# Kernel tuning notes

Measured on AMD Instinct MI355X. Metric: run time of the kernel, lower is better.

Reference implementation:

```python
import jax, jax.numpy as jnp
import numpy as np

N = 4096      # mesh nodes (seq len)
D = 512       # input_dim_nodes / hidden_size
F = 512       # ffn_hidden_size (hidden_dim)
NH = 4        # num_attention_heads
HD = D // NH  # head dim = 128
L = 2         # processor_layers
EPS = 1e-5
SCALE = 1.0 / float(np.sqrt(HD))
NEG = -1e9


def setup_inputs() -> dict:
    key = jax.random.key(0)
    ks = jax.random.split(key, 16)
    nfeat = jax.random.normal(ks[0], (N, D), jnp.float32)
    # sparse graph adjacency mask: True = masked out (TE 'arbitrary' convention)
    mask = jax.random.uniform(ks[1], (N, N)) < 0.99
    idx = jnp.arange(N)
    mask = mask.at[idx, idx].set(False)  # keep self-edges unmasked
    s = 0.02
    p = lambda k, shape: jax.random.normal(k, shape, jnp.float32) * s
    return dict(
        nfeat=nfeat, mask=mask,
        ln1_g=jnp.ones((L, D), jnp.float32), ln1_b=jnp.zeros((L, D), jnp.float32),
        wq=p(ks[2], (L, D, D)), bq=p(ks[3], (L, D)),
        wk=p(ks[4], (L, D, D)), bk=p(ks[5], (L, D)),
        wv=p(ks[6], (L, D, D)), bv=p(ks[7], (L, D)),
        wo=p(ks[8], (L, D, D)), bo=p(ks[9], (L, D)),
        ln2_g=jnp.ones((L, D), jnp.float32), ln2_b=jnp.zeros((L, D), jnp.float32),
        fc1_w=p(ks[10], (L, F, D)), fc1_b=p(ks[11], (L, F)),
        fc2_w=p(ks[12], (L, D, F)), fc2_b=p(ks[13], (L, D)),
    )


def _ln(x, g, b):
    mu = x.mean(-1, keepdims=True)
    var = ((x - mu) ** 2).mean(-1, keepdims=True)
    return (x - mu) * jax.lax.rsqrt(var + EPS) * g + b


def reference(nfeat, mask, ln1_g, ln1_b, wq, bq, wk, bk, wv, bv, wo, bo,
              ln2_g, ln2_b, fc1_w, fc1_b, fc2_w, fc2_b):
    def layer(x, p):
        g1, b1, Wq, Bq, Wk, Bk, Wv, Bv, Wo, Bo, g2, b2, W1, B1, W2, B2 = p
        # --- pre-LN self-attention with arbitrary mask ---
        h = _ln(x, g1, b1)                                  # [N, D]
        q = (h @ Wq.T + Bq).reshape(N, NH, HD)
        k = (h @ Wk.T + Bk).reshape(N, NH, HD)
        v = (h @ Wv.T + Bv).reshape(N, NH, HD)
        scores = jnp.einsum('qhd,khd->hqk', q, k) * SCALE   # [NH, N, N]
        scores = jnp.where(mask[None], NEG, scores)
        attn = jax.nn.softmax(scores, axis=-1)
        o = jnp.einsum('hqk,khd->qhd', attn, v).reshape(N, D)
        x = x + o @ Wo.T + Bo
        # --- pre-LN MLP ---
        h2 = _ln(x, g2, b2)
        m = jax.nn.gelu(h2 @ W1.T + B1, approximate=False) @ W2.T + B2
        return x + m, None

    xs = (ln1_g, ln1_b, wq, bq, wk, bk, wv, bv, wo, bo,
          ln2_g, ln2_b, fc1_w, fc1_b, fc2_w, fc2_b)
    out, _ = jax.lax.scan(layer, nfeat, xs)
    return out
```

## Files before the change

### kernel.cpp

```cpp
#include <hip/hip_runtime.h>
#include <math.h>

#define NN 4096
#define DD 512
#define FF 512
#define CAP 256
#define SCALE 0.08838834764831845f

typedef __attribute__((ext_vector_type(8))) short short8;
typedef __attribute__((ext_vector_type(8))) unsigned short ushort8;
typedef __attribute__((ext_vector_type(4))) float floatx4;

__device__ __forceinline__ float bf2f(unsigned short u) {
    union { unsigned int i; float f; } x; x.i = ((unsigned int)u) << 16; return x.f;
}
__device__ __forceinline__ unsigned short f2bf(float f) {
    union { float f; unsigned int i; } x; x.f = f;
    unsigned int r = (x.i + 0x7FFFu + ((x.i >> 16) & 1u)) >> 16;
    return (unsigned short)r;
}
__device__ __forceinline__ void gld_lds16(const void* g, void* l) {
    __builtin_amdgcn_global_load_lds((const __attribute__((address_space(1))) void*)g,
                                     (__attribute__((address_space(3))) void*)l, 16, 0, 0);
}

__global__ void build_idx_kernel(const int* __restrict__ mask,
                                 int* __restrict__ idx, int* __restrict__ cnt) {
    int row = blockIdx.x;
    __shared__ int c;
    if (threadIdx.x == 0) c = 0;
    __syncthreads();
    const int4* mrow = (const int4*)(mask + (size_t)row * NN);
    for (int j4 = threadIdx.x; j4 < NN / 4; j4 += blockDim.x) {
        int4 m4 = mrow[j4];
        int base = j4 * 4;
        if (m4.x == 0) idx[row * CAP + atomicAdd(&c, 1)] = base;
        if (m4.y == 0) idx[row * CAP + atomicAdd(&c, 1)] = base + 1;
        if (m4.z == 0) idx[row * CAP + atomicAdd(&c, 1)] = base + 2;
        if (m4.w == 0) idx[row * CAP + atomicAdd(&c, 1)] = base + 3;
    }
    __syncthreads();
    if (threadIdx.x == 0) cnt[row] = (c < CAP) ? c : CAP;
}

struct FoldArgs {
    const float* w[6];
    const float* bias[6];
    const float* ln1_g; const float* ln1_b;
    const float* ln2_g; const float* ln2_b;
};
__global__ void fold_weights(FoldArgs fa, unsigned short* __restrict__ wc,
                             float* __restrict__ c0, float* __restrict__ c1) {
    int r = blockIdx.y;
    int l = r / 6, m = r - l * 6;
    int wave = threadIdx.x >> 6, lane = threadIdx.x & 63;
    int n = blockIdx.x * 4 + wave;

    const float* wrow = fa.w[m] + (size_t)l * DD * DD + (size_t)n * DD;
    float4 w0 = *(const float4*)&wrow[lane * 8];
    float4 w1 = *(const float4*)&wrow[lane * 8 + 4];
    float we[8] = {w0.x, w0.y, w0.z, w0.w, w1.x, w1.y, w1.z, w1.w};

    bool folded = (m < 3) || (m == 4);
    float s1 = 0.f, sb = 0.f;
    float wg[8];
    if (folded) {
        const float* gp = (m < 3) ? fa.ln1_g + l * DD : fa.ln2_g + l * DD;
        const float* bp = (m < 3) ? fa.ln1_b + l * DD : fa.ln2_b + l * DD;
        float4 g0 = *(const float4*)&gp[lane * 8];
        float4 g1 = *(const float4*)&gp[lane * 8 + 4];
        float4 b0 = *(const float4*)&bp[lane * 8];
        float4 b1 = *(const float4*)&bp[lane * 8 + 4];
        float ge[8] = {g0.x, g0.y, g0.z, g0.w, g1.x, g1.y, g1.z, g1.w};
        float be[8] = {b0.x, b0.y, b0.z, b0.w, b1.x, b1.y, b1.z, b1.w};
#pragma unroll
        for (int e = 0; e < 8; e++) {
            wg[e] = we[e] * ge[e];
            s1 += wg[e];
            sb += we[e] * be[e];
        }
    } else {
#pragma unroll
        for (int e = 0; e < 8; e++) wg[e] = we[e];
    }
    ushort8 ov;
#pragma unroll
    for (int e = 0; e < 8; e++) ov[e] = f2bf(wg[e]);
    *(ushort8*)&wc[(size_t)r * DD * DD + (size_t)n * DD + lane * 8] = ov;

    if (folded) {
#pragma unroll
        for (int off = 32; off; off >>= 1) { s1 += __shfl_xor(s1, off); sb += __shfl_xor(sb, off); }
    }
    if (lane == 0) {
        c1[r * DD + n] = folded ? s1 : 0.f;
        c0[r * DD + n] = (folded ? sb : 0.f) + fa.bias[m][l * DD + n];
    }
}

__global__ void init_stats(const float* __restrict__ x, unsigned short* __restrict__ xb,
                           float* __restrict__ S) {
    int wave = threadIdx.x >> 6, lane = threadIdx.x & 63;
    int row = blockIdx.x * 4 + wave;
    const float* xr = x + (size_t)row * DD;
    float4 p0 = *(const float4*)&xr[lane * 8];
    float4 p1 = *(const float4*)&xr[lane * 8 + 4];
    float v[8] = {p0.x, p0.y, p0.z, p0.w, p1.x, p1.y, p1.z, p1.w};
    float s = 0.f, q = 0.f;
    ushort8 ov;
#pragma unroll
    for (int e = 0; e < 8; e++) { s += v[e]; q += v[e] * v[e]; ov[e] = f2bf(v[e]); }
#pragma unroll
    for (int off = 32; off; off >>= 1) { s += __shfl_xor(s, off); q += __shfl_xor(q, off); }
    *(ushort8*)&xb[(size_t)row * DD + lane * 8] = ov;
    if (lane == 0) { S[2 * row] = s; S[2 * row + 1] = q; }
}

__global__ void zero_kernel(float* __restrict__ p, int n) {
    int i = blockIdx.x * blockDim.x + threadIdx.x;
    if (i < n) p[i] = 0.f;
}

template <int MODE>
__launch_bounds__(256)
__global__ void gemm_bf16(const unsigned short* __restrict__ A, const unsigned short* __restrict__ B,
                          const float* __restrict__ c0, const float* __restrict__ c1,
                          const float* __restrict__ statsIn, const float* __restrict__ resIn,
                          float* __restrict__ resOut, unsigned short* __restrict__ outB,
                          float* __restrict__ statsOut, int M, int Nout, int K) {
    __shared__ unsigned short As[64 * 32];
    __shared__ unsigned short Bs[64 * 32];
    const int m0 = blockIdx.y * 64, n0 = blockIdx.x * 64;
    const int t = threadIdx.x;
    const int wave = t >> 6, lane = t & 63;
    const int wm = (wave & 1) * 32, wn = (wave >> 1) * 32;
    const int srow = t >> 2, scol = (t & 3) * 8;
    const int fr = lane & 15, fq = (lane >> 4) * 8;

    floatx4 acc[2][2] = {};

    const unsigned short* ag = A + (size_t)(m0 + srow) * K + scol;
    const unsigned short* bg = B + (size_t)(n0 + srow) * K + scol;
    unsigned short* as = As + t * 8;
    unsigned short* bs = Bs + t * 8;

    for (int k0 = 0; k0 < K; k0 += 32) {
        __syncthreads();
        gld_lds16(ag + k0, as);
        gld_lds16(bg + k0, bs);
        __syncthreads();
        short8 af[2], bf[2];
#pragma unroll
        for (int i = 0; i < 2; i++)
            af[i] = *(const short8*)&As[(wm + 16 * i + fr) * 32 + fq];
#pragma unroll
        for (int j = 0; j < 2; j++)
            bf[j] = *(const short8*)&Bs[(wn + 16 * j + fr) * 32 + fq];
#pragma unroll
        for (int i = 0; i < 2; i++)
#pragma unroll
            for (int j = 0; j < 2; j++)
                acc[i][j] = __builtin_amdgcn_mfma_f32_16x16x32_bf16(af[i], bf[j], acc[i][j], 0, 0, 0);
    }

    const int er = (lane >> 4) * 4, ec = lane & 15;
    int colj[2]; float c0v[2], c1v[2];
#pragma unroll
    for (int j = 0; j < 2; j++) {
        colj[j] = n0 + wn + 16 * j + ec;
        c0v[j] = c0[colj[j]];
        if (MODE < 2) c1v[j] = c1[colj[j]];
    }

#pragma unroll
    for (int i = 0; i < 2; i++) {
#pragma unroll
        for (int r = 0; r < 4; r++) {
            int row = m0 + wm + 16 * i + er + r;
            if (MODE < 2) {
                float s = statsIn[2 * row], q = statsIn[2 * row + 1];
                float mu = s * (1.0f / DD);
                float var = q * (1.0f / DD) - mu * mu;
                float rm = rsqrtf(var + 1e-5f);
                float rmu = rm * mu;
#pragma unroll
                for (int j = 0; j < 2; j++) {
                    float val = rm * acc[i][j][r] - rmu * c1v[j] + c0v[j];
                    if (MODE == 1) val = 0.5f * val * (1.0f + erff(val * 0.70710678118654752f));
                    outB[(size_t)row * Nout + colj[j]] = f2bf(val);
                }
            } else {
                float xn[2];
#pragma unroll
                for (int j = 0; j < 2; j++) {
                    xn[j] = resIn[(size_t)row * Nout + colj[j]] + acc[i][j][r] + c0v[j];
                    resOut[(size_t)row * Nout + colj[j]] = xn[j];
                    if (MODE == 2) outB[(size_t)row * Nout + colj[j]] = f2bf(xn[j]);
                }
                if (MODE == 2) {
                    float s = xn[0] + xn[1];
                    float q = xn[0] * xn[0] + xn[1] * xn[1];
#pragma unroll
                    for (int off = 1; off < 16; off <<= 1) {
                        s += __shfl_xor(s, off);
                        q += __shfl_xor(q, off);
                    }
                    if ((lane & 15) == 0) {
                        atomicAdd(&statsOut[2 * row], s);
                        atomicAdd(&statsOut[2 * row + 1], q);
                    }
                }
            }
        }
    }
}

__global__ void sparse_attn(const unsigned short* __restrict__ qkv, const int* __restrict__ idx,
                            const int* __restrict__ cnt, unsigned short* __restrict__ o) {
    int wave = threadIdx.x >> 6, lane = threadIdx.x & 63;
    int qslot = wave >> 1, half = wave & 1;
    int qi = blockIdx.x * 4 + qslot;
    __shared__ float obuf[4][64][8];
    __shared__ float sbuf[4][64];

    ushort8 qv = *(const ushort8*)(qkv + (size_t)qi * 1536 + lane * 8);
    float qf[8];
#pragma unroll
    for (int e = 0; e < 8; e++) qf[e] = bf2f(qv[e]);

    int c = cnt[qi];
    const int* ir = idx + qi * CAP;
    float sum = 0.f, oa[8] = {};

    for (int j = half; j < c; j += 2) {
        int kj = ir[j];
        const unsigned short* kv_base = qkv + (size_t)kj * 1536;
        ushort8 kv = *(const ushort8*)(kv_base + 512 + lane * 8);
        ushort8 vv = *(const ushort8*)(kv_base + 1024 + lane * 8);
        float d = 0.f;
#pragma unroll
        for (int e = 0; e < 8; e++) d += qf[e] * bf2f(kv[e]);
        d += __shfl_xor(d, 1);
        d += __shfl_xor(d, 2);
        d += __shfl_xor(d, 4);
        d += __shfl_xor(d, 8);
        float p = __expf(d * SCALE);
        sum += p;
#pragma unroll
        for (int e = 0; e < 8; e++) oa[e] += p * bf2f(vv[e]);
    }

    if (half == 1) {
#pragma unroll
        for (int e = 0; e < 8; e++) obuf[qslot][lane][e] = oa[e];
        sbuf[qslot][lane] = sum;
    }
    __syncthreads();
    if (half == 0) {
        sum += sbuf[qslot][lane];
        float inv = 1.0f / sum;
        ushort8 ov;
#pragma unroll
        for (int e = 0; e < 8; e++) ov[e] = f2bf((oa[e] + obuf[qslot][lane][e]) * inv);
        *(ushort8*)(o + (size_t)qi * 512 + lane * 8) = ov;
    }
}

extern "C" void kernel_launch(void* const* d_in, const int* in_sizes, int n_in,
                              void* d_out, int out_size, void* d_ws, size_t ws_size,
                              hipStream_t stream) {
    const float* nfeat = (const float*)d_in[0];
    const int*   mask  = (const int*)d_in[1];
    const float* ln1_g = (const float*)d_in[2];
    const float* ln1_b = (const float*)d_in[3];
    const float* wq    = (const float*)d_in[4];
    const float* bq    = (const float*)d_in[5];
    const float* wk    = (const float*)d_in[6];
    const float* bk    = (const float*)d_in[7];
    const float* wv    = (const float*)d_in[8];
    const float* bv    = (const float*)d_in[9];
    const float* wo    = (const float*)d_in[10];
    const float* bo    = (const float*)d_in[11];
    const float* ln2_g = (const float*)d_in[12];
    const float* ln2_b = (const float*)d_in[13];
    const float* fc1_w = (const float*)d_in[14];
    const float* fc1_b = (const float*)d_in[15];
    const float* fc2_w = (const float*)d_in[16];
    const float* fc2_b = (const float*)d_in[17];

    const size_t ND = (size_t)NN * DD;
    float* x            = (float*)d_ws;
    unsigned short* xb  = (unsigned short*)(x + ND);
    unsigned short* qkv = xb + ND;
    unsigned short* o   = qkv + (size_t)NN * 1536;
    unsigned short* m1  = o + ND;
    unsigned short* wc  = m1 + ND;
    float* c0           = (float*)(wc + (size_t)12 * DD * DD);
    float* c1           = c0 + 12 * DD;
    float* S            = c1 + 12 * DD;
    int*   idx          = (int*)(S + 4 * NN * 2);
    int*   cnt          = idx + (size_t)NN * CAP;

    FoldArgs fa;
    fa.w[0] = wq; fa.w[1] = wk; fa.w[2] = wv; fa.w[3] = wo; fa.w[4] = fc1_w; fa.w[5] = fc2_w;
    fa.bias[0] = bq; fa.bias[1] = bk; fa.bias[2] = bv; fa.bias[3] = bo; fa.bias[4] = fc1_b; fa.bias[5] = fc2_b;
    fa.ln1_g = ln1_g; fa.ln1_b = ln1_b; fa.ln2_g = ln2_g; fa.ln2_b = ln2_b;

    fold_weights<<<dim3(128, 12), 256, 0, stream>>>(fa, wc, c0, c1);
    build_idx_kernel<<<NN, 256, 0, stream>>>(mask, idx, cnt);
    init_stats<<<NN / 4, 256, 0, stream>>>(nfeat, xb, S);
    zero_kernel<<<24, 1024, 0, stream>>>(S + NN * 2, 3 * NN * 2);

    for (int l = 0; l < 2; l++) {
        unsigned short* wl = wc + (size_t)l * 6 * DD * DD;
        float* cl0 = c0 + l * 6 * DD;
        float* cl1 = c1 + l * 6 * DD;
        float* Sa = S + (size_t)(2 * l) * NN * 2;
        float* Sb = S + (size_t)(2 * l + 1) * NN * 2;
        const float* resIn0 = (l == 0) ? nfeat : x;

        gemm_bf16<0><<<dim3(24, 64), 256, 0, stream>>>(xb, wl, cl0, cl1, Sa,
                                                       nullptr, nullptr, qkv, nullptr, NN, 1536, DD);
        sparse_attn<<<NN / 4, 512, 0, stream>>>(qkv, idx, cnt, o);
        gemm_bf16<2><<<dim3(8, 64), 256, 0, stream>>>(o, wl + (size_t)3 * DD * DD, cl0 + 3 * DD, nullptr,
                                                      nullptr, resIn0, x, xb, Sb, NN, DD, DD);
        gemm_bf16<1><<<dim3(8, 64), 256, 0, stream>>>(xb, wl + (size_t)4 * DD * DD, cl0 + 4 * DD, cl1 + 4 * DD, Sb,
                                                      nullptr, nullptr, m1, nullptr, NN, FF, DD);
        if (l == 0) {
            gemm_bf16<2><<<dim3(8, 64), 256, 0, stream>>>(m1, wl + (size_t)5 * DD * DD, cl0 + 5 * DD, nullptr,
                                                          nullptr, x, x, xb, S + (size_t)2 * NN * 2, NN, DD, FF);
        } else {
            gemm_bf16<3><<<dim3(8, 64), 256, 0, stream>>>(m1, wl + (size_t)5 * DD * DD, cl0 + 5 * DD, nullptr,
                                                          nullptr, x, (float*)d_out, nullptr, nullptr, NN, DD, FF);
        }
    }
}
```

Baseline: 321.8 us.

## Fuse all stages into one cooperative persistent kernel with grid syncs

Replaces the chain of separate launches (weight fold, mask indexing, stats init, zeroing, GEMMs, attention) with one cooperative kernel of 512 blocks that walks every stage and separates them with grid.sync(). Row statistics are no longer accumulated with global atomics. Each GEMM column block writes partial sums to a buffer, and the next GEMM reduces them when it loads its LayerNorm coefficients into shared memory, which also removes the zeroing kernel. The aim is to cut launch and tail overhead. The cost is less parallelism in the QKV GEMM (1536 tiles on 512 blocks) and attention, plus the grid-wide barriers themselves. A multi-launch fallback runs if the cooperative launch fails.

```diff
diff --git a/kernel.cpp b/kernel.cpp
--- a/kernel.cpp
+++ b/kernel.cpp
@@ -1,5 +1,8 @@
 #include <hip/hip_runtime.h>
+#include <hip/hip_cooperative_groups.h>
 #include <math.h>
+
+namespace cg = cooperative_groups;
 
 #define NN 4096
 #define DD 512
@@ -7,155 +10,159 @@
 #define CAP 256
 #define SCALE 0.08838834764831845f
 
+typedef unsigned short u16;
 typedef __attribute__((ext_vector_type(8))) short short8;
 typedef __attribute__((ext_vector_type(8))) unsigned short ushort8;
 typedef __attribute__((ext_vector_type(4))) float floatx4;
 
-__device__ __forceinline__ float bf2f(unsigned short u) {
+__device__ __forceinline__ float bf2f(u16 u) {
     union { unsigned int i; float f; } x; x.i = ((unsigned int)u) << 16; return x.f;
 }
-__device__ __forceinline__ unsigned short f2bf(float f) {
+__device__ __forceinline__ u16 f2bf(float f) {
     union { float f; unsigned int i; } x; x.f = f;
     unsigned int r = (x.i + 0x7FFFu + ((x.i >> 16) & 1u)) >> 16;
-    return (unsigned short)r;
+    return (u16)r;
 }
 __device__ __forceinline__ void gld_lds16(const void* g, void* l) {
     __builtin_amdgcn_global_load_lds((const __attribute__((address_space(1))) void*)g,
                                      (__attribute__((address_space(3))) void*)l, 16, 0, 0);
 }
 
-__global__ void build_idx_kernel(const int* __restrict__ mask,
-                                 int* __restrict__ idx, int* __restrict__ cnt) {
-    int row = blockIdx.x;
-    __shared__ int c;
-    if (threadIdx.x == 0) c = 0;
+struct KArgs {
+    const float* nfeat; const int* mask;
+    const float* ln1_g; const float* ln1_b; const float* ln2_g; const float* ln2_b;
+    const float* w[6]; const float* bias[6];
+    float* x; u16* xb; u16* qkv; u16* o; u16* m1;
+    u16* wc; float* c0; float* c1; float* S0; float* P;
+    int* idx; int* cnt; float* out;
+};
+
+
+__device__ void setup_body(const KArgs& a, int bid, int t, int* cbar) {
+    const int wave = t >> 6, lane = t & 63;
+    for (int it = 0; it < 3; it++) {
+        int gid = bid * 3 + it;
+        int r = gid >> 7, nb = gid & 127;
+        int l = r / 6, m = r - l * 6;
+        int n = nb * 4 + wave;
+        const float* wrow = a.w[m] + (size_t)l * DD * DD + (size_t)n * DD;
+        float4 w0 = *(const float4*)&wrow[lane * 8];
+        float4 w1 = *(const float4*)&wrow[lane * 8 + 4];
+        float we[8] = {w0.x, w0.y, w0.z, w0.w, w1.x, w1.y, w1.z, w1.w};
+        bool folded = (m < 3) || (m == 4);
+        float s1 = 0.f, sb = 0.f, wg[8];
+        if (folded) {
+            const float* gp = (m < 3) ? a.ln1_g + l * DD : a.ln2_g + l * DD;
+            const float* bp = (m < 3) ? a.ln1_b + l * DD : a.ln2_b + l * DD;
+            float4 g0 = *(const float4*)&gp[lane * 8];
+            float4 g1 = *(const float4*)&gp[lane * 8 + 4];
+            float4 b0 = *(const float4*)&bp[lane * 8];
+            float4 b1 = *(const float4*)&bp[lane * 8 + 4];
+            float ge[8] = {g0.x, g0.y, g0.z, g0.w, g1.x, g1.y, g1.z, g1.w};
+            float be[8] = {b0.x, b0.y, b0.z, b0.w, b1.x, b1.y, b1.z, b1.w};
+#pragma unroll
+            for (int e = 0; e < 8; e++) { wg[e] = we[e] * ge[e]; s1 += wg[e]; sb += we[e] * be[e]; }
+        } else {
+#pragma unroll
+            for (int e = 0; e < 8; e++) wg[e] = we[e];
+        }
+        ushort8 ov;
+#pragma unroll
+        for (int e = 0; e < 8; e++) ov[e] = f2bf(wg[e]);
+        *(ushort8*)&a.wc[(size_t)r * DD * DD + (size_t)n * DD + lane * 8] = ov;
+        if (folded) {
+#pragma unroll
+            for (int off = 32; off; off >>= 1) { s1 += __shfl_xor(s1, off); sb += __shfl_xor(sb, off); }
+        }
+        if (lane == 0) {
+            a.c1[r * DD + n] = folded ? s1 : 0.f;
+            a.c0[r * DD + n] = (folded ? sb : 0.f) + a.bias[m][l * DD + n];
+        }
+    }
+    if (t < 8) cbar[t] = 0;
     __syncthreads();
-    const int4* mrow = (const int4*)(mask + (size_t)row * NN);
-    for (int j4 = threadIdx.x; j4 < NN / 4; j4 += blockDim.x) {
-        int4 m4 = mrow[j4];
-        int base = j4 * 4;
-        if (m4.x == 0) idx[row * CAP + atomicAdd(&c, 1)] = base;
-        if (m4.y == 0) idx[row * CAP + atomicAdd(&c, 1)] = base + 1;
-        if (m4.z == 0) idx[row * CAP + atomicAdd(&c, 1)] = base + 2;
-        if (m4.w == 0) idx[row * CAP + atomicAdd(&c, 1)] = base + 3;
+    for (int h = 0; h < 2; h++) {
+        int rr = wave * 2 + h;
+        int row = bid * 8 + rr;
+        const int4* mr = (const int4*)(a.mask + (size_t)row * NN);
+        for (int j4 = lane; j4 < NN / 4; j4 += 64) {
+            int4 m4 = mr[j4];
+            int base = j4 * 4;
+            if (m4.x == 0) { int p = atomicAdd(&cbar[rr], 1); if (p < CAP) a.idx[row * CAP + p] = base; }
+            if (m4.y == 0) { int p = atomicAdd(&cbar[rr], 1); if (p < CAP) a.idx[row * CAP + p] = base + 1; }
+            if (m4.z == 0) { int p = atomicAdd(&cbar[rr], 1); if (p < CAP) a.idx[row * CAP + p] = base + 2; }
+            if (m4.w == 0) { int p = atomicAdd(&cbar[rr], 1); if (p < CAP) a.idx[row * CAP + p] = base + 3; }
+        }
     }
     __syncthreads();
-    if (threadIdx.x == 0) cnt[row] = (c < CAP) ? c : CAP;
-}
-
-struct FoldArgs {
-    const float* w[6];
-    const float* bias[6];
-    const float* ln1_g; const float* ln1_b;
-    const float* ln2_g; const float* ln2_b;
-};
-__global__ void fold_weights(FoldArgs fa, unsigned short* __restrict__ wc,
-                             float* __restrict__ c0, float* __restrict__ c1) {
-    int r = blockIdx.y;
-    int l = r / 6, m = r - l * 6;
-    int wave = threadIdx.x >> 6, lane = threadIdx.x & 63;
-    int n = blockIdx.x * 4 + wave;
-
-    const float* wrow = fa.w[m] + (size_t)l * DD * DD + (size_t)n * DD;
-    float4 w0 = *(const float4*)&wrow[lane * 8];
-    float4 w1 = *(const float4*)&wrow[lane * 8 + 4];
-    float we[8] = {w0.x, w0.y, w0.z, w0.w, w1.x, w1.y, w1.z, w1.w};
-
-    bool folded = (m < 3) || (m == 4);
-    float s1 = 0.f, sb = 0.f;
-    float wg[8];
-    if (folded) {
-        const float* gp = (m < 3) ? fa.ln1_g + l * DD : fa.ln2_g + l * DD;
-        const float* bp = (m < 3) ? fa.ln1_b + l * DD : fa.ln2_b + l * DD;
-        float4 g0 = *(const float4*)&gp[lane * 8];
-        float4 g1 = *(const float4*)&gp[lane * 8 + 4];
-        float4 b0 = *(const float4*)&bp[lane * 8];
-        float4 b1 = *(const float4*)&bp[lane * 8 + 4];
-        float ge[8] = {g0.x, g0.y, g0.z, g0.w, g1.x, g1.y, g1.z, g1.w};
-        float be[8] = {b0.x, b0.y, b0.z, b0.w, b1.x, b1.y, b1.z, b1.w};
-#pragma unroll
-        for (int e = 0; e < 8; e++) {
-            wg[e] = we[e] * ge[e];
-            s1 += wg[e];
-            sb += we[e] * be[e];
-        }
-    } else {
-#pragma unroll
-        for (int e = 0; e < 8; e++) wg[e] = we[e];
-    }
-    ushort8 ov;
-#pragma unroll
-    for (int e = 0; e < 8; e++) ov[e] = f2bf(wg[e]);
-    *(ushort8*)&wc[(size_t)r * DD * DD + (size_t)n * DD + lane * 8] = ov;
-
-    if (folded) {
-#pragma unroll
-        for (int off = 32; off; off >>= 1) { s1 += __shfl_xor(s1, off); sb += __shfl_xor(sb, off); }
-    }
-    if (lane == 0) {
-        c1[r * DD + n] = folded ? s1 : 0.f;
-        c0[r * DD + n] = (folded ? sb : 0.f) + fa.bias[m][l * DD + n];
-    }
-}
-
-__global__ void init_stats(const float* __restrict__ x, unsigned short* __restrict__ xb,
-                           float* __restrict__ S) {
-    int wave = threadIdx.x >> 6, lane = threadIdx.x & 63;
-    int row = blockIdx.x * 4 + wave;
-    const float* xr = x + (size_t)row * DD;
-    float4 p0 = *(const float4*)&xr[lane * 8];
-    float4 p1 = *(const float4*)&xr[lane * 8 + 4];
-    float v[8] = {p0.x, p0.y, p0.z, p0.w, p1.x, p1.y, p1.z, p1.w};
-    float s = 0.f, q = 0.f;
-    ushort8 ov;
-#pragma unroll
-    for (int e = 0; e < 8; e++) { s += v[e]; q += v[e] * v[e]; ov[e] = f2bf(v[e]); }
-#pragma unroll
-    for (int off = 32; off; off >>= 1) { s += __shfl_xor(s, off); q += __shfl_xor(q, off); }
-    *(ushort8*)&xb[(size_t)row * DD + lane * 8] = ov;
-    if (lane == 0) { S[2 * row] = s; S[2 * row + 1] = q; }
-}
-
-__global__ void zero_kernel(float* __restrict__ p, int n) {
-    int i = blockIdx.x * blockDim.x + threadIdx.x;
-    if (i < n) p[i] = 0.f;
+    if (t < 8) { int c = cbar[t]; a.cnt[bid * 8 + t] = (c < CAP) ? c : CAP; }
+    for (int h = 0; h < 2; h++) {
+        int row = bid * 8 + wave + h * 4;
+        const float* xr = a.nfeat + (size_t)row * DD;
+        float4 p0 = *(const float4*)&xr[lane * 8];
+        float4 p1 = *(const float4*)&xr[lane * 8 + 4];
+        float v[8] = {p0.x, p0.y, p0.z, p0.w, p1.x, p1.y, p1.z, p1.w};
+        float s = 0.f, q = 0.f;
+        ushort8 ov;
+#pragma unroll
+        for (int e = 0; e < 8; e++) { s += v[e]; q += v[e] * v[e]; ov[e] = f2bf(v[e]); }
+#pragma unroll
+        for (int off = 32; off; off >>= 1) { s += __shfl_xor(s, off); q += __shfl_xor(q, off); }
+        *(ushort8*)&a.xb[(size_t)row * DD + lane * 8] = ov;
+        if (lane == 0) { a.S0[2 * row] = s; a.S0[2 * row + 1] = q; }
+    }
 }
 
 template <int MODE>
-__launch_bounds__(256)
-__global__ void gemm_bf16(const unsigned short* __restrict__ A, const unsigned short* __restrict__ B,
+__device__ void gemm_body(const u16* __restrict__ A, const u16* __restrict__ B,
                           const float* __restrict__ c0, const float* __restrict__ c1,
-                          const float* __restrict__ statsIn, const float* __restrict__ resIn,
-                          float* __restrict__ resOut, unsigned short* __restrict__ outB,
-                          float* __restrict__ statsOut, int M, int Nout, int K) {
-    __shared__ unsigned short As[64 * 32];
-    __shared__ unsigned short Bs[64 * 32];
-    const int m0 = blockIdx.y * 64, n0 = blockIdx.x * 64;
-    const int t = threadIdx.x;
+                          const float* __restrict__ Sfin, const float* __restrict__ Ppart,
+                          const float* __restrict__ resIn, float* __restrict__ resOut,
+                          u16* __restrict__ outB, float* __restrict__ Ppout,
+                          int bx, int by, int Nout, int t,
+                          u16* As, u16* Bs, float* lnA, float* lnB, float (*ssc)[2][2]) {
     const int wave = t >> 6, lane = t & 63;
+    const int m0 = by * 64, n0 = bx * 64;
     const int wm = (wave & 1) * 32, wn = (wave >> 1) * 32;
     const int srow = t >> 2, scol = (t & 3) * 8;
     const int fr = lane & 15, fq = (lane >> 4) * 8;
 
+    if (MODE < 2) {
+        if (t < 64) {
+            int row = m0 + t;
+            float s, q;
+            if (Sfin) { s = Sfin[2 * row]; q = Sfin[2 * row + 1]; }
+            else {
+                s = 0.f; q = 0.f;
+#pragma unroll
+                for (int p = 0; p < 8; p++) {
+                    s += Ppart[((size_t)p * NN + row) * 2];
+                    q += Ppart[((size_t)p * NN + row) * 2 + 1];
+                }
+            }
+            float mu = s * (1.0f / DD);
+            float var = q * (1.0f / DD) - mu * mu;
+            float rm = rsqrtf(var + 1e-5f);
+            lnA[t] = rm; lnB[t] = rm * mu;
+        }
+    }
+
     floatx4 acc[2][2] = {};
-
-    const unsigned short* ag = A + (size_t)(m0 + srow) * K + scol;
-    const unsigned short* bg = B + (size_t)(n0 + srow) * K + scol;
-    unsigned short* as = As + t * 8;
-    unsigned short* bs = Bs + t * 8;
-
-    for (int k0 = 0; k0 < K; k0 += 32) {
+    const u16* ag = A + (size_t)(m0 + srow) * DD + scol;
+    const u16* bg = B + (size_t)(n0 + srow) * DD + scol;
+    u16* as = As + t * 8;
+    u16* bs = Bs + t * 8;
+
+    for (int k0 = 0; k0 < DD; k0 += 32) {
         __syncthreads();
         gld_lds16(ag + k0, as);
         gld_lds16(bg + k0, bs);
         __syncthreads();
         short8 af[2], bf[2];
 #pragma unroll
-        for (int i = 0; i < 2; i++)
-            af[i] = *(const short8*)&As[(wm + 16 * i + fr) * 32 + fq];
-#pragma unroll
-        for (int j = 0; j < 2; j++)
-            bf[j] = *(const short8*)&Bs[(wn + 16 * j + fr) * 32 + fq];
+        for (int i = 0; i < 2; i++) af[i] = *(const short8*)&As[(wm + 16 * i + fr) * 32 + fq];
+#pragma unroll
+        for (int j = 0; j < 2; j++) bf[j] = *(const short8*)&Bs[(wn + 16 * j + fr) * 32 + fq];
 #pragma unroll
         for (int i = 0; i < 2; i++)
 #pragma unroll
@@ -176,13 +183,10 @@
     for (int i = 0; i < 2; i++) {
 #pragma unroll
         for (int r = 0; r < 4; r++) {
-            int row = m0 + wm + 16 * i + er + r;
+            int rowL = wm + 16 * i + er + r;
+            int row = m0 + rowL;
             if (MODE < 2) {
-                float s = statsIn[2 * row], q = statsIn[2 * row + 1];
-                float mu = s * (1.0f / DD);
-                float var = q * (1.0f / DD) - mu * mu;
-                float rm = rsqrtf(var + 1e-5f);
-                float rmu = rm * mu;
+                float rm = lnA[rowL], rmu = lnB[rowL];
 #pragma unroll
                 for (int j = 0; j < 2; j++) {
                     float val = rm * acc[i][j][r] - rmu * c1v[j] + c0v[j];
@@ -201,137 +205,215 @@
                     float s = xn[0] + xn[1];
                     float q = xn[0] * xn[0] + xn[1] * xn[1];
 #pragma unroll
-                    for (int off = 1; off < 16; off <<= 1) {
-                        s += __shfl_xor(s, off);
-                        q += __shfl_xor(q, off);
-                    }
-                    if ((lane & 15) == 0) {
-                        atomicAdd(&statsOut[2 * row], s);
-                        atomicAdd(&statsOut[2 * row + 1], q);
-                    }
+                    for (int off = 1; off < 16; off <<= 1) { s += __shfl_xor(s, off); q += __shfl_xor(q, off); }
+                    if ((lane & 15) == 0) { ssc[rowL][wn >> 5][0] = s; ssc[rowL][wn >> 5][1] = q; }
                 }
             }
         }
     }
-}
-
-__global__ void sparse_attn(const unsigned short* __restrict__ qkv, const int* __restrict__ idx,
-                            const int* __restrict__ cnt, unsigned short* __restrict__ o) {
-    int wave = threadIdx.x >> 6, lane = threadIdx.x & 63;
-    int qslot = wave >> 1, half = wave & 1;
-    int qi = blockIdx.x * 4 + qslot;
-    __shared__ float obuf[4][64][8];
-    __shared__ float sbuf[4][64];
-
-    ushort8 qv = *(const ushort8*)(qkv + (size_t)qi * 1536 + lane * 8);
-    float qf[8];
-#pragma unroll
-    for (int e = 0; e < 8; e++) qf[e] = bf2f(qv[e]);
-
-    int c = cnt[qi];
-    const int* ir = idx + qi * CAP;
-    float sum = 0.f, oa[8] = {};
-
-    for (int j = half; j < c; j += 2) {
-        int kj = ir[j];
-        const unsigned short* kv_base = qkv + (size_t)kj * 1536;
-        ushort8 kv = *(const ushort8*)(kv_base + 512 + lane * 8);
-        ushort8 vv = *(const ushort8*)(kv_base + 1024 + lane * 8);
-        float d = 0.f;
-#pragma unroll
-        for (int e = 0; e < 8; e++) d += qf[e] * bf2f(kv[e]);
-        d += __shfl_xor(d, 1);
-        d += __shfl_xor(d, 2);
-        d += __shfl_xor(d, 4);
-        d += __shfl_xor(d, 8);
-        float p = __expf(d * SCALE);
-        sum += p;
-#pragma unroll
-        for (int e = 0; e < 8; e++) oa[e] += p * bf2f(vv[e]);
-    }
-
-    if (half == 1) {
-#pragma unroll
-        for (int e = 0; e < 8; e++) obuf[qslot][lane][e] = oa[e];
-        sbuf[qslot][lane] = sum;
-    }
-    __syncthreads();
-    if (half == 0) {
-        sum += sbuf[qslot][lane];
-        float inv = 1.0f / sum;
-        ushort8 ov;
-#pragma unroll
-        for (int e = 0; e < 8; e++) ov[e] = f2bf((oa[e] + obuf[qslot][lane][e]) * inv);
-        *(ushort8*)(o + (size_t)qi * 512 + lane * 8) = ov;
-    }
+    if (MODE == 2) {
+        __syncthreads();
+        if (t < 64) {
+            float s = ssc[t][0][0] + ssc[t][1][0];
+            float q = ssc[t][0][1] + ssc[t][1][1];
+            Ppout[((size_t)bx * NN + m0 + t) * 2] = s;
+            Ppout[((size_t)bx * NN + m0 + t) * 2 + 1] = q;
+        }
+    }
+}
+
+__device__ void attn_body(const u16* __restrict__ qkv, const int* __restrict__ idx,
+                          const int* __restrict__ cnt, u16* __restrict__ o,
+                          int bid, int t, float (*obuf)[64][8], float (*sbuf)[64]) {
+    const int wave = t >> 6, lane = t & 63;
+    const int qslot = wave >> 1, half = wave & 1;
+    for (int it = 0; it < 4; it++) {
+        __syncthreads();
+        int qi = bid * 8 + it * 2 + qslot;
+        ushort8 qv = *(const ushort8*)(qkv + (size_t)qi * 1536 + lane * 8);
+        float qf[8];
+#pragma unroll
+        for (int e = 0; e < 8; e++) qf[e] = bf2f(qv[e]);
+        int c = cnt[qi];
+        const int* ir = idx + qi * CAP;
+        float sum = 0.f, oa[8] = {};
+        for (int j = half; j < c; j += 2) {
+            int kj = ir[j];
+            const u16* kv_base = qkv + (size_t)kj * 1536;
+            ushort8 kv = *(const ushort8*)(kv_base + 512 + lane * 8);
+            ushort8 vv = *(const ushort8*)(kv_base + 1024 + lane * 8);
+            float d = 0.f;
+#pragma unroll
+            for (int e = 0; e < 8; e++) d += qf[e] * bf2f(kv[e]);
+            d += __shfl_xor(d, 1);
+            d += __shfl_xor(d, 2);
+            d += __shfl_xor(d, 4);
+            d += __shfl_xor(d, 8);
+            float p = __expf(d * SCALE);
+            sum += p;
+#pragma unroll
+            for (int e = 0; e < 8; e++) oa[e] += p * bf2f(vv[e]);
+        }
+        if (half == 1) {
+#pragma unroll
+            for (int e = 0; e < 8; e++) obuf[qslot][lane][e] = oa[e];
+            sbuf[qslot][lane] = sum;
+        }
+        __syncthreads();
+        if (half == 0) {
+            sum += sbuf[qslot][lane];
+            float inv = 1.0f / sum;
+            ushort8 ov;
+#pragma unroll
+            for (int e = 0; e < 8; e++) ov[e] = f2bf((oa[e] + obuf[qslot][lane][e]) * inv);
+            *(ushort8*)(o + (size_t)qi * 512 + lane * 8) = ov;
+        }
+    }
+}
+
+#define MEGA_SHARED \
+    __shared__ u16 As[64 * 32]; \
+    __shared__ u16 Bs[64 * 32]; \
+    __shared__ float lnA[64], lnB[64]; \
+    __shared__ float ssc[64][2][2]; \
+    __shared__ float obuf[2][64][8]; \
+    __shared__ float sbuf[2][64]; \
+    __shared__ int cbar[8];
+
+__launch_bounds__(256, 2)
+__global__ void mega(KArgs a) {
+    MEGA_SHARED
+    cg::grid_group grid = cg::this_grid();
+    const int bid = blockIdx.x, t = threadIdx.x;
+
+    setup_body(a, bid, t, cbar);
+    grid.sync();
+
+    for (int l = 0; l < 2; l++) {
+        const u16* wl = a.wc + (size_t)l * 6 * DD * DD;
+        const float* cl0 = a.c0 + l * 6 * DD;
+        const float* cl1 = a.c1 + l * 6 * DD;
+        const float* Sfin = (l == 0) ? a.S0 : nullptr;
+
+        for (int it = 0; it < 3; it++) {
+            int tid2 = it * 512 + bid;
+            int bx = tid2 % 24, by = tid2 / 24;
+            __syncthreads();
+            gemm_body<0>(a.xb, wl, cl0, cl1, Sfin, a.P, nullptr, nullptr, a.qkv, nullptr,
+                         bx, by, 1536, t, As, Bs, lnA, lnB, ssc);
+        }
+        grid.sync();
+
+        attn_body(a.qkv, a.idx, a.cnt, a.o, bid, t, obuf, sbuf);
+        grid.sync();
+
+        gemm_body<2>(a.o, wl + (size_t)3 * DD * DD, cl0 + 3 * DD, nullptr, nullptr, nullptr,
+                     (l == 0) ? a.nfeat : a.x, a.x, a.xb, a.P,
+                     bid & 7, bid >> 3, DD, t, As, Bs, lnA, lnB, ssc);
+        grid.sync();
+
+        gemm_body<1>(a.xb, wl + (size_t)4 * DD * DD, cl0 + 4 * DD, cl1 + 4 * DD, nullptr, a.P,
+                     nullptr, nullptr, a.m1, nullptr,
+                     bid & 7, bid >> 3, FF, t, As, Bs, lnA, lnB, ssc);
+        grid.sync();
+
+        if (l == 0) {
+            gemm_body<2>(a.m1, wl + (size_t)5 * DD * DD, cl0 + 5 * DD, nullptr, nullptr, nullptr,
+                         a.x, a.x, a.xb, a.P,
+                         bid & 7, bid >> 3, DD, t, As, Bs, lnA, lnB, ssc);
+            grid.sync();
+        } else {
+            gemm_body<3>(a.m1, wl + (size_t)5 * DD * DD, cl0 + 5 * DD, nullptr, nullptr, nullptr,
+                         a.x, a.out, nullptr, nullptr,
+                         bid & 7, bid >> 3, DD, t, As, Bs, lnA, lnB, ssc);
+        }
+    }
+}
+
+__launch_bounds__(256, 2)
+__global__ void setup_kernel(KArgs a) {
+    __shared__ int cbar[8];
+    setup_body(a, blockIdx.x, threadIdx.x, cbar);
+}
+
+template <int MODE>
+__launch_bounds__(256, 2)
+__global__ void gemm_stage(const u16* A, const u16* B, const float* c0, const float* c1,
+                           const float* Sfin, const float* Ppart, const float* resIn,
+                           float* resOut, u16* outB, float* Ppout, int ntx, int Nout) {
+    __shared__ u16 As[64 * 32];
+    __shared__ u16 Bs[64 * 32];
+    __shared__ float lnA[64], lnB[64];
+    __shared__ float ssc[64][2][2];
+    int bx = blockIdx.x % ntx, by = blockIdx.x / ntx;
+    gemm_body<MODE>(A, B, c0, c1, Sfin, Ppart, resIn, resOut, outB, Ppout,
+                    bx, by, Nout, threadIdx.x, As, Bs, lnA, lnB, ssc);
+}
+
+__launch_bounds__(256, 2)
+__global__ void attn_stage(const u16* qkv, const int* idx, const int* cnt, u16* o) {
+    __shared__ float obuf[2][64][8];
+    __shared__ float sbuf[2][64];
+    attn_body(qkv, idx, cnt, o, blockIdx.x, threadIdx.x, obuf, sbuf);
 }
 
 extern "C" void kernel_launch(void* const* d_in, const int* in_sizes, int n_in,
                               void* d_out, int out_size, void* d_ws, size_t ws_size,
                               hipStream_t stream) {
-    const float* nfeat = (const float*)d_in[0];
-    const int*   mask  = (const int*)d_in[1];
-    const float* ln1_g = (const float*)d_in[2];
-    const float* ln1_b = (const float*)d_in[3];
-    const float* wq    = (const float*)d_in[4];
-    const float* bq    = (const float*)d_in[5];
-    const float* wk    = (const float*)d_in[6];
-    const float* bk    = (const float*)d_in[7];
-    const float* wv    = (const float*)d_in[8];
-    const float* bv    = (const float*)d_in[9];
-    const float* wo    = (const float*)d_in[10];
-    const float* bo    = (const float*)d_in[11];
-    const float* ln2_g = (const float*)d_in[12];
-    const float* ln2_b = (const float*)d_in[13];
-    const float* fc1_w = (const float*)d_in[14];
-    const float* fc1_b = (const float*)d_in[15];
-    const float* fc2_w = (const float*)d_in[16];
-    const float* fc2_b = (const float*)d_in[17];
+    KArgs a;
+    a.nfeat = (const float*)d_in[0];
+    a.mask  = (const int*)d_in[1];
+    a.ln1_g = (const float*)d_in[2];
+    a.ln1_b = (const float*)d_in[3];
+    a.w[0] = (const float*)d_in[4];  a.bias[0] = (const float*)d_in[5];
+    a.w[1] = (const float*)d_in[6];  a.bias[1] = (const float*)d_in[7];
+    a.w[2] = (const float*)d_in[8];  a.bias[2] = (const float*)d_in[9];
+    a.w[3] = (const float*)d_in[10]; a.bias[3] = (const float*)d_in[11];
+    a.ln2_g = (const float*)d_in[12];
+    a.ln2_b = (const float*)d_in[13];
+    a.w[4] = (const float*)d_in[14]; a.bias[4] = (const float*)d_in[15];
+    a.w[5] = (const float*)d_in[16]; a.bias[5] = (const float*)d_in[17];
 
     const size_t ND = (size_t)NN * DD;
-    float* x            = (float*)d_ws;
-    unsigned short* xb  = (unsigned short*)(x + ND);
-    unsigned short* qkv = xb + ND;
-    unsigned short* o   = qkv + (size_t)NN * 1536;
-    unsigned short* m1  = o + ND;
-    unsigned short* wc  = m1 + ND;
-    float* c0           = (float*)(wc + (size_t)12 * DD * DD);
-    float* c1           = c0 + 12 * DD;
-    float* S            = c1 + 12 * DD;
-    int*   idx          = (int*)(S + 4 * NN * 2);
-    int*   cnt          = idx + (size_t)NN * CAP;
-
-    FoldArgs fa;
-    fa.w[0] = wq; fa.w[1] = wk; fa.w[2] = wv; fa.w[3] = wo; fa.w[4] = fc1_w; fa.w[5] = fc2_w;
-    fa.bias[0] = bq; fa.bias[1] = bk; fa.bias[2] = bv; fa.bias[3] = bo; fa.bias[4] = fc1_b; fa.bias[5] = fc2_b;
-    fa.ln1_g = ln1_g; fa.ln1_b = ln1_b; fa.ln2_g = ln2_g; fa.ln2_b = ln2_b;
-
-    fold_weights<<<dim3(128, 12), 256, 0, stream>>>(fa, wc, c0, c1);
-    build_idx_kernel<<<NN, 256, 0, stream>>>(mask, idx, cnt);
-    init_stats<<<NN / 4, 256, 0, stream>>>(nfeat, xb, S);
-    zero_kernel<<<24, 1024, 0, stream>>>(S + NN * 2, 3 * NN * 2);
-
-    for (int l = 0; l < 2; l++) {
-        unsigned short* wl = wc + (size_t)l * 6 * DD * DD;
-        float* cl0 = c0 + l * 6 * DD;
-        float* cl1 = c1 + l * 6 * DD;
-        float* Sa = S + (size_t)(2 * l) * NN * 2;
-        float* Sb = S + (size_t)(2 * l + 1) * NN * 2;
-        const float* resIn0 = (l == 0) ? nfeat : x;
-
-        gemm_bf16<0><<<dim3(24, 64), 256, 0, stream>>>(xb, wl, cl0, cl1, Sa,
-                                                       nullptr, nullptr, qkv, nullptr, NN, 1536, DD);
-        sparse_attn<<<NN / 4, 512, 0, stream>>>(qkv, idx, cnt, o);
-        gemm_bf16<2><<<dim3(8, 64), 256, 0, stream>>>(o, wl + (size_t)3 * DD * DD, cl0 + 3 * DD, nullptr,
-                                                      nullptr, resIn0, x, xb, Sb, NN, DD, DD);
-        gemm_bf16<1><<<dim3(8, 64), 256, 0, stream>>>(xb, wl + (size_t)4 * DD * DD, cl0 + 4 * DD, cl1 + 4 * DD, Sb,
-                                                      nullptr, nullptr, m1, nullptr, NN, FF, DD);
-        if (l == 0) {
-            gemm_bf16<2><<<dim3(8, 64), 256, 0, stream>>>(m1, wl + (size_t)5 * DD * DD, cl0 + 5 * DD, nullptr,
-                                                          nullptr, x, x, xb, S + (size_t)2 * NN * 2, NN, DD, FF);
-        } else {
-            gemm_bf16<3><<<dim3(8, 64), 256, 0, stream>>>(m1, wl + (size_t)5 * DD * DD, cl0 + 5 * DD, nullptr,
-                                                          nullptr, x, (float*)d_out, nullptr, nullptr, NN, DD, FF);
-        }
-    }
-}
+    a.x   = (float*)d_ws;
+    a.xb  = (u16*)(a.x + ND);
+    a.qkv = a.xb + ND;
+    a.o   = a.qkv + (size_t)NN * 1536;
+    a.m1  = a.o + ND;
+    a.wc  = a.m1 + ND;
+    a.c0  = (float*)(a.wc + (size_t)12 * DD * DD);
+    a.c1  = a.c0 + 12 * DD;
+    a.S0  = a.c1 + 12 * DD;
+    a.P   = a.S0 + (size_t)NN * 2;
+    a.idx = (int*)(a.P + (size_t)8 * NN * 2);
+    a.cnt = a.idx + (size_t)NN * CAP;
+    a.out = (float*)d_out;
+
+    void* params[] = {(void*)&a};
+    hipError_t err = hipLaunchCooperativeKernel((const void*)mega, dim3(512), dim3(256),
+                                                params, 0, stream);
+    if (err != hipSuccess) {
+        setup_kernel<<<512, 256, 0, stream>>>(a);
+        for (int l = 0; l < 2; l++) {
+            const u16* wl = a.wc + (size_t)l * 6 * DD * DD;
+            const float* cl0 = a.c0 + l * 6 * DD;
+            const float* cl1 = a.c1 + l * 6 * DD;
+            const float* Sfin = (l == 0) ? a.S0 : nullptr;
+            gemm_stage<0><<<1536, 256, 0, stream>>>(a.xb, wl, cl0, cl1, Sfin, a.P,
+                                                    nullptr, nullptr, a.qkv, nullptr, 24, 1536);
+            attn_stage<<<512, 256, 0, stream>>>(a.qkv, a.idx, a.cnt, a.o);
+            gemm_stage<2><<<512, 256, 0, stream>>>(a.o, wl + (size_t)3 * DD * DD, cl0 + 3 * DD, nullptr,
+                                                   nullptr, nullptr, (l == 0) ? a.nfeat : a.x,
+                                                   a.x, a.xb, a.P, 8, DD);
+            gemm_stage<1><<<512, 256, 0, stream>>>(a.xb, wl + (size_t)4 * DD * DD, cl0 + 4 * DD, cl1 + 4 * DD,
+                                                   nullptr, a.P, nullptr, nullptr, a.m1, nullptr, 8, FF);
+            if (l == 0) {
+                gemm_stage<2><<<512, 256, 0, stream>>>(a.m1, wl + (size_t)5 * DD * DD, cl0 + 5 * DD, nullptr,
+                                                       nullptr, nullptr, a.x, a.x, a.xb, a.P, 8, DD);
+            } else {
+                gemm_stage<3><<<512, 256, 0, stream>>>(a.m1, wl + (size_t)5 * DD * DD, cl0 + 5 * DD, nullptr,
+                                                       nullptr, nullptr, a.x, a.out, nullptr, nullptr, 8, DD);
+            }
+        }
+    }
+}
```

Result: slower. 1.002 ms (+211.3%).
